# Kernel tuning notes

Hardware: AMD Instinct MI355X
Metric: run time of the kernel (lower is better)

The kernel has to match this reference:

```python
import jax, jax.numpy as jnp
import numpy as np

HIDDEN = 1024
INTER = 4096
NUM_EXPERTS = 8
TOP_K = 2


def setup_inputs() -> dict:
    key = jax.random.key(0)
    ks = jax.random.split(key, 6)
    B, S = 4, 2048
    hidden_states = jax.random.normal(ks[0], (B, S, HIDDEN), dtype=jnp.float32)
    scale = 0.02
    # nn.Linear stores weight as [out, in]; y = x @ W.T + b
    gate_w = jax.random.normal(ks[1], (NUM_EXPERTS, HIDDEN), dtype=jnp.float32) * scale
    W1 = jax.random.normal(ks[2], (NUM_EXPERTS, INTER, HIDDEN), dtype=jnp.float32) * scale
    b1 = jax.random.normal(ks[3], (NUM_EXPERTS, INTER), dtype=jnp.float32) * scale
    W2 = jax.random.normal(ks[4], (NUM_EXPERTS, HIDDEN, INTER), dtype=jnp.float32) * scale
    b2 = jax.random.normal(ks[5], (NUM_EXPERTS, HIDDEN), dtype=jnp.float32) * scale
    return {"hidden_states": hidden_states, "gate_w": gate_w,
            "W1": W1, "b1": b1, "W2": W2, "b2": b2}


def reference(hidden_states, gate_w, W1, b1, W2, b2):
    B, S, H = hidden_states.shape
    x = hidden_states.reshape(-1, H)                      # [T, H]
    # Gating: top-k logits -> softmax over the k selected experts only
    gate_logits = x @ gate_w.T                            # [T, E]
    top_vals, top_idx = jax.lax.top_k(gate_logits, TOP_K) # [T, K]
    weights = jax.nn.softmax(top_vals, axis=-1)           # [T, K]
    # Per-token combine weight for each expert (0 if not selected)
    one_hot = jax.nn.one_hot(top_idx, NUM_EXPERTS, dtype=x.dtype)  # [T, K, E]
    combine = jnp.einsum("tk,tke->te", weights, one_hot)           # [T, E]
    # Expert MLPs: fixed small loop over experts (structurally distinct params)
    out = jnp.zeros_like(x)
    for e in range(NUM_EXPERTS):
        h = jax.nn.gelu(x @ W1[e].T + b1[e], approximate=False)  # [T, INTER]
        y = h @ W2[e].T + b2[e]                                   # [T, H]
        out = out + combine[:, e:e + 1] * y
    return out.reshape(B, S, H)
```

## Files before the change

kernel.cpp:

```cpp
#include <hip/hip_runtime.h>
#include <hip/hip_bf16.h>
#include <stdint.h>

#define HID 1024
#define INTER_ 4096
#define NE 8
#define NTOK 8192
#define NPAIR (NTOK * 2)
#define MAXT 72

using f32x4 = __attribute__((ext_vector_type(4))) float;
using bf16x8 = __attribute__((ext_vector_type(8))) __bf16;
using ushort8v = __attribute__((ext_vector_type(8))) unsigned short;

__device__ __forceinline__ unsigned short f2b(float f) {
  unsigned int u = __float_as_uint(f);
  u += 0x7fffu + ((u >> 16) & 1u);
  return (unsigned short)(u >> 16);
}
__device__ __forceinline__ float b2f(unsigned short u) {
  return __uint_as_float((unsigned int)u << 16);
}

__device__ __forceinline__ float gelu_f(float v) {
  float z = fabsf(v) * 0.70710678118654752f;
  float t = __builtin_amdgcn_rcpf(1.f + 0.3275911f * z);
  float p = t * (0.254829592f +
            t * (-0.284496736f +
            t * (1.421413741f +
            t * (-1.453152027f + t * 1.061405429f))));
  float er = 1.f - p * __expf(-z * z);
  er = copysignf(er, v);
  return 0.5f * v * (1.f + er);
}

#define GLD_LDS(gp, lp)                                                        \
  __builtin_amdgcn_global_load_lds(                                            \
      (const __attribute__((address_space(1))) unsigned int*)(const void*)(gp),\
      (__attribute__((address_space(3))) unsigned int*)(void*)(lp), 16, 0, 0)

#define WAITV(N) asm volatile("s_waitcnt vmcnt(" #N ")" ::: "memory")

__global__ __launch_bounds__(256) void gate_kernel(
    const float* __restrict__ x, const float* __restrict__ gw,
    int* __restrict__ topi, float* __restrict__ topw,
    unsigned short* __restrict__ xb)
{
  int gwave = (blockIdx.x * 256 + threadIdx.x) >> 6;
  int lane = threadIdx.x & 63;
  if (gwave >= NTOK) return;
  const float* xr = x + (size_t)gwave * HID;
  unsigned short* xo = xb + (size_t)gwave * HID;
  float acc[NE];
#pragma unroll
  for (int e = 0; e < NE; ++e) acc[e] = 0.f;
#pragma unroll
  for (int q = 0; q < 4; ++q) {
    float4 v = *reinterpret_cast<const float4*>(xr + q * 256 + lane * 4);
    ushort4 uv;
    uv.x = f2b(v.x); uv.y = f2b(v.y); uv.z = f2b(v.z); uv.w = f2b(v.w);
    *reinterpret_cast<ushort4*>(xo + q * 256 + lane * 4) = uv;
#pragma unroll
    for (int e = 0; e < NE; ++e) {
      float4 wv = *reinterpret_cast<const float4*>(gw + e * HID + q * 256 + lane * 4);
      acc[e] += v.x * wv.x + v.y * wv.y + v.z * wv.z + v.w * wv.w;
    }
  }
#pragma unroll
  for (int e = 0; e < NE; ++e) {
#pragma unroll
    for (int off = 32; off > 0; off >>= 1) acc[e] += __shfl_xor(acc[e], off);
  }
  if (lane == 0) {
    float v0 = -1e30f; int i0 = 0;
#pragma unroll
    for (int e = 0; e < NE; ++e) if (acc[e] > v0) { v0 = acc[e]; i0 = e; }
    float v1 = -1e30f; int i1 = 0;
#pragma unroll
    for (int e = 0; e < NE; ++e) if (e != i0 && acc[e] > v1) { v1 = acc[e]; i1 = e; }
    float e1 = __expf(v1 - v0);
    float s = 1.f + e1;
    topi[gwave * 2] = i0; topi[gwave * 2 + 1] = i1;
    topw[gwave * 2] = 1.f / s; topw[gwave * 2 + 1] = e1 / s;
  }
}

__global__ __launch_bounds__(256) void hist_kernel(const int* __restrict__ topi,
                                                   int* __restrict__ bcnt)
{
  int tid = threadIdx.x, blk = blockIdx.x;
  int t = blk * 256 + tid;
  int e0 = topi[t * 2], e1 = topi[t * 2 + 1];
  int w = tid >> 6, lane = tid & 63;
  __shared__ int wcnt[4][NE];
#pragma unroll
  for (int e = 0; e < NE; ++e) {
    unsigned long long m0 = __ballot(e0 == e);
    unsigned long long m1 = __ballot(e1 == e);
    if (lane == 0) wcnt[w][e] = __popcll(m0) + __popcll(m1);
  }
  __syncthreads();
  if (tid < NE) {
    int s = 0;
#pragma unroll
    for (int w2 = 0; w2 < 4; ++w2) s += wcnt[w2][tid];
    bcnt[blk * NE + tid] = s;
  }
}

__global__ void scan2_kernel(const int* __restrict__ bcnt, int* __restrict__ offs,
                             int* __restrict__ tile_e, int* __restrict__ tile_m,
                             int* __restrict__ ntile, int* __restrict__ gbase)
{
  __shared__ int cnts[NE];
  __shared__ int soffs[NE];
  int tid = threadIdx.x;
  if (tid < NE) {
    int s = 0;
#pragma unroll
    for (int b = 0; b < 32; ++b) s += bcnt[b * NE + tid];
    cnts[tid] = s;
  }
  __syncthreads();
  if (tid == 0) {
    int o = 0, tt = 0;
    for (int e = 0; e < NE; ++e) {
      offs[e] = o; soffs[e] = o;
      int c = cnts[e];
      for (int m = 0; m < c; m += 256) { tile_e[tt] = e; tile_m[tt] = m; ++tt; }
      o += c;
    }
    offs[NE] = o;
    *ntile = tt;
  }
  __syncthreads();
  if (tid < 32 * NE) {
    int b = tid >> 3, e = tid & 7;
    int g = soffs[e];
    for (int b2 = 0; b2 < b; ++b2) g += bcnt[b2 * NE + e];
    gbase[b * NE + e] = g;
  }
}

__global__ __launch_bounds__(256) void scatter2_kernel(
    const int* __restrict__ topi, const float* __restrict__ topw,
    const int* __restrict__ gbase,
    int* __restrict__ toklist, float* __restrict__ wlist, int* __restrict__ pos)
{
  int tid = threadIdx.x, blk = blockIdx.x;
  int t = blk * 256 + tid;
  int e0 = topi[t * 2], e1 = topi[t * 2 + 1];
  float w0 = topw[t * 2], w1 = topw[t * 2 + 1];
  int w = tid >> 6, lane = tid & 63;
  unsigned long long lt = (1ull << lane) - 1ull;
  unsigned long long le = lt | (1ull << lane);
  __shared__ int wcnt[4][NE];
  __shared__ int wbase[4][NE];
  int r0 = 0, r1 = 0;
#pragma unroll
  for (int e = 0; e < NE; ++e) {
    unsigned long long m0 = __ballot(e0 == e);
    unsigned long long m1 = __ballot(e1 == e);
    if (lane == 0) wcnt[w][e] = __popcll(m0) + __popcll(m1);
    if (e0 == e) r0 = __popcll(m0 & lt) + __popcll(m1 & lt);
    if (e1 == e) r1 = __popcll(m0 & le) + __popcll(m1 & lt);
  }
  __syncthreads();
  if (tid < 4 * NE) {
    int w2 = tid >> 3, e = tid & 7;
    int b = gbase[blk * NE + e];
    for (int w3 = 0; w3 < w2; ++w3) b += wcnt[w3][e];
    wbase[w2][e] = b;
  }
  __syncthreads();
  int P0 = wbase[w][e0] + r0;
  int P1 = wbase[w][e1] + r1;
  toklist[P0] = t; wlist[P0] = w0; pos[t * 2] = P0;
  toklist[P1] = t; wlist[P1] = w1; pos[t * 2 + 1] = P1;
}

__global__ __launch_bounds__(256) void cvtw_kernel(
    const float* __restrict__ W1, const float* __restrict__ W2,
    unsigned short* __restrict__ w1b, unsigned short* __restrict__ w2b, int n8)
{
  int half = gridDim.x >> 1;
  const float* src = (blockIdx.x < half) ? W1 : W2;
  unsigned short* dst = (blockIdx.x < half) ? w1b : w2b;
  int b0 = (blockIdx.x < half) ? blockIdx.x : blockIdx.x - half;
  int stride = half * 256;
  for (int i = b0 * 256 + threadIdx.x; i < n8; i += stride) {
    const float4* s = reinterpret_cast<const float4*>(src) + (size_t)i * 2;
    float4 a = s[0], b = s[1];
    ushort8v u;
    u[0] = f2b(a.x); u[1] = f2b(a.y); u[2] = f2b(a.z); u[3] = f2b(a.w);
    u[4] = f2b(b.x); u[5] = f2b(b.y); u[6] = f2b(b.z); u[7] = f2b(b.w);
    reinterpret_cast<ushort8v*>(dst)[i] = u;
  }
}


__global__ __launch_bounds__(512, 4) void gemm1_kernel(
    const unsigned short* __restrict__ xb, const unsigned short* __restrict__ w1b,
    const float* __restrict__ b1,
    const int* __restrict__ toklist, const int* __restrict__ offs,
    const int* __restrict__ tile_e, const int* __restrict__ tile_m,
    const int* __restrict__ ntile,
    unsigned short* __restrict__ hb)
{
  const int t = blockIdx.y;
  if (t >= *ntile) return;
  const int e = tile_e[t];
  const int m0 = tile_m[t];
  const int base = offs[e];
  const int cnt = offs[e + 1] - base;
  const int n0 = blockIdx.x * 128;

  __shared__ __align__(16) unsigned short As[3][256 * 32];
  __shared__ __align__(16) unsigned short Bs[3][128 * 32];

  const int tid = threadIdx.x;
  const int lane = tid & 63;
  const int w = tid >> 6;
  const int wr = w >> 1, wc = w & 1;

  const int r0 = tid >> 2;
  const int sl = tid & 3;
  const int scg = sl ^ ((r0 >> 1) & 3);
  const unsigned short* gA[2];
  const unsigned short* gB;
#pragma unroll
  for (int g = 0; g < 2; ++g) {
    int row = g * 128 + r0;
    int mrow = m0 + row; if (mrow >= cnt) mrow = cnt - 1;
    int tk = toklist[base + mrow];
    gA[g] = xb + (size_t)tk * HID + scg * 8;
  }
  gB = w1b + ((size_t)e * INTER_ + n0 + r0) * HID + scg * 8;

  int raq[4], rbq[4];
#pragma unroll
  for (int i = 0; i < 4; ++i) {
    int rA = wr * 64 + i * 16 + (lane & 15);
    raq[i] = rA * 32 + (((lane >> 4) ^ ((rA >> 1) & 3)) * 8);
    int rB = wc * 64 + i * 16 + (lane & 15);
    rbq[i] = rB * 32 + (((lane >> 4) ^ ((rB >> 1) & 3)) * 8);
  }

  f32x4 acc[4][4];
#pragma unroll
  for (int i = 0; i < 4; ++i)
#pragma unroll
    for (int j = 0; j < 4; ++j) acc[i][j] = (f32x4){0.f, 0.f, 0.f, 0.f};

  auto stage = [&](int slot, int s) {
    const int kof = s * 32;
    GLD_LDS(gA[0] + kof, &As[slot][tid * 8]);
    GLD_LDS(gA[1] + kof, &As[slot][4096 + tid * 8]);
    GLD_LDS(gB + kof,    &Bs[slot][tid * 8]);
  };
  auto compute = [&](int slot) {
    const unsigned short* Ab = &As[slot][0];
    const unsigned short* Bb = &Bs[slot][0];
    bf16x8 bfr[4];
#pragma unroll
    for (int j = 0; j < 4; ++j) bfr[j] = *reinterpret_cast<const bf16x8*>(Bb + rbq[j]);
#pragma unroll
    for (int i = 0; i < 4; ++i) {
      bf16x8 af = *reinterpret_cast<const bf16x8*>(Ab + raq[i]);
#pragma unroll
      for (int j = 0; j < 4; ++j)
        acc[i][j] = __builtin_amdgcn_mfma_f32_16x16x32_bf16(af, bfr[j], acc[i][j], 0, 0, 0);
    }
  };

  const int NS = HID / 32;
  stage(0, 0); stage(1, 1);
#pragma unroll 3
  for (int s = 0; s < NS - 2; ++s) {
    WAITV(3);
    __builtin_amdgcn_s_barrier();
    stage((s + 2) % 3, s + 2);
    compute(s % 3);
  }
  WAITV(3); __builtin_amdgcn_s_barrier(); compute((NS - 2) % 3);
  WAITV(0); __builtin_amdgcn_s_barrier(); compute((NS - 1) % 3);

  float bias[4];
  const int colb = n0 + wc * 64 + (lane & 15);
#pragma unroll
  for (int j = 0; j < 4; ++j) bias[j] = b1[(size_t)e * INTER_ + colb + j * 16];
#pragma unroll
  for (int i = 0; i < 4; ++i) {
    int mbase = m0 + wr * 64 + i * 16 + (lane >> 4) * 4;
#pragma unroll
    for (int r = 0; r < 4; ++r) {
      int m = mbase + r;
      if (m < cnt) {
        unsigned short* hrow = hb + (size_t)(base + m) * INTER_ + colb;
#pragma unroll
        for (int j = 0; j < 4; ++j)
          hrow[j * 16] = f2b(gelu_f(acc[i][j][r] + bias[j]));
      }
    }
  }
}

__global__ __launch_bounds__(512, 4) void gemm2_kernel(
    const unsigned short* __restrict__ hb, const unsigned short* __restrict__ w2b,
    const int* __restrict__ offs,
    const int* __restrict__ tile_e, const int* __restrict__ tile_m,
    const int* __restrict__ ntile,
    unsigned short* __restrict__ part)
{
  const int t = blockIdx.y;
  if (t >= *ntile) return;
  const int e = tile_e[t];
  const int m0 = tile_m[t];
  const int base = offs[e];
  const int cnt = offs[e + 1] - base;
  const int n0 = blockIdx.x * 128;
  const int kbase = blockIdx.z * (INTER_ / 2);

  __shared__ __align__(16) unsigned short As[3][256 * 32];
  __shared__ __align__(16) unsigned short Bs[3][128 * 32];

  const int tid = threadIdx.x;
  const int lane = tid & 63;
  const int w = tid >> 6;
  const int wr = w >> 1, wc = w & 1;

  const int r0 = tid >> 2;
  const int sl = tid & 3;
  const int scg = sl ^ ((r0 >> 1) & 3);
  const unsigned short* gA[2];
  const unsigned short* gB;
#pragma unroll
  for (int g = 0; g < 2; ++g) {
    int row = g * 128 + r0;
    int mrow = m0 + row; if (mrow >= cnt) mrow = cnt - 1;
    gA[g] = hb + (size_t)(base + mrow) * INTER_ + kbase + scg * 8;
  }
  gB = w2b + ((size_t)e * HID + n0 + r0) * INTER_ + kbase + scg * 8;

  int raq[4], rbq[4];
#pragma unroll
  for (int i = 0; i < 4; ++i) {
    int rA = wr * 64 + i * 16 + (lane & 15);
    raq[i] = rA * 32 + (((lane >> 4) ^ ((rA >> 1) & 3)) * 8);
    int rB = wc * 64 + i * 16 + (lane & 15);
    rbq[i] = rB * 32 + (((lane >> 4) ^ ((rB >> 1) & 3)) * 8);
  }

  f32x4 acc[4][4];
#pragma unroll
  for (int i = 0; i < 4; ++i)
#pragma unroll
    for (int j = 0; j < 4; ++j) acc[i][j] = (f32x4){0.f, 0.f, 0.f, 0.f};

  auto stage = [&](int slot, int s) {
    const int kof = s * 32;
    GLD_LDS(gA[0] + kof, &As[slot][tid * 8]);
    GLD_LDS(gA[1] + kof, &As[slot][4096 + tid * 8]);
    GLD_LDS(gB + kof,    &Bs[slot][tid * 8]);
  };
  auto compute = [&](int slot) {
    const unsigned short* Ab = &As[slot][0];
    const unsigned short* Bb = &Bs[slot][0];
    bf16x8 bfr[4];
#pragma unroll
    for (int j = 0; j < 4; ++j) bfr[j] = *reinterpret_cast<const bf16x8*>(Bb + rbq[j]);
#pragma unroll
    for (int i = 0; i < 4; ++i) {
      bf16x8 af = *reinterpret_cast<const bf16x8*>(Ab + raq[i]);
#pragma unroll
      for (int j = 0; j < 4; ++j)
        acc[i][j] = __builtin_amdgcn_mfma_f32_16x16x32_bf16(af, bfr[j], acc[i][j], 0, 0, 0);
    }
  };

  const int NS = (INTER_ / 2) / 32;
  stage(0, 0); stage(1, 1);
#pragma unroll 3
  for (int s = 0; s < NS - 2; ++s) {
    WAITV(3);
    __builtin_amdgcn_s_barrier();
    stage((s + 2) % 3, s + 2);
    compute(s % 3);
  }
  WAITV(3); __builtin_amdgcn_s_barrier(); compute((NS - 2) % 3);
  WAITV(0); __builtin_amdgcn_s_barrier(); compute((NS - 1) % 3);

  const int colb = n0 + wc * 64 + (lane & 15);
  unsigned short* pbase = part + (size_t)blockIdx.z * NPAIR * HID;
#pragma unroll
  for (int i = 0; i < 4; ++i) {
    int mbase = m0 + wr * 64 + i * 16 + (lane >> 4) * 4;
#pragma unroll
    for (int r = 0; r < 4; ++r) {
      int m = mbase + r;
      if (m < cnt) {
        unsigned short* prow = pbase + (size_t)(base + m) * HID + colb;
#pragma unroll
        for (int j = 0; j < 4; ++j)
          prow[j * 16] = f2b(acc[i][j][r]);
      }
    }
  }
}

__global__ __launch_bounds__(256) void combine_kernel(
    const unsigned short* __restrict__ part, const float* __restrict__ b2,
    const int* __restrict__ topi, const float* __restrict__ topw,
    const int* __restrict__ pos, float* __restrict__ out)
{
  int t = blockIdx.x * 4 + (threadIdx.x >> 6);
  int lane = threadIdx.x & 63;
  int c0 = lane * 16;
  float o[16];
#pragma unroll
  for (int c = 0; c < 16; ++c) o[c] = 0.f;
#pragma unroll
  for (int k = 0; k < 2; ++k) {
    int p = pos[t * 2 + k];
    int e = topi[t * 2 + k];
    float wk = topw[t * 2 + k];
    const unsigned short* rp0 = part + (size_t)p * HID + c0;
    const unsigned short* rp1 = part + ((size_t)NPAIR + p) * HID + c0;
    const float* bb = b2 + (size_t)e * HID + c0;
#pragma unroll
    for (int v = 0; v < 2; ++v) {
      ushort8v a = *reinterpret_cast<const ushort8v*>(rp0 + v * 8);
      ushort8v b = *reinterpret_cast<const ushort8v*>(rp1 + v * 8);
      float4 bb0 = *reinterpret_cast<const float4*>(bb + v * 8);
      float4 bb1 = *reinterpret_cast<const float4*>(bb + v * 8 + 4);
      o[v * 8 + 0] += wk * (b2f(a[0]) + b2f(b[0]) + bb0.x);
      o[v * 8 + 1] += wk * (b2f(a[1]) + b2f(b[1]) + bb0.y);
      o[v * 8 + 2] += wk * (b2f(a[2]) + b2f(b[2]) + bb0.z);
      o[v * 8 + 3] += wk * (b2f(a[3]) + b2f(b[3]) + bb0.w);
      o[v * 8 + 4] += wk * (b2f(a[4]) + b2f(b[4]) + bb1.x);
      o[v * 8 + 5] += wk * (b2f(a[5]) + b2f(b[5]) + bb1.y);
      o[v * 8 + 6] += wk * (b2f(a[6]) + b2f(b[6]) + bb1.z);
      o[v * 8 + 7] += wk * (b2f(a[7]) + b2f(b[7]) + bb1.w);
    }
  }
  float4* op = reinterpret_cast<float4*>(out + (size_t)t * HID + c0);
#pragma unroll
  for (int v = 0; v < 4; ++v)
    op[v] = make_float4(o[v * 4], o[v * 4 + 1], o[v * 4 + 2], o[v * 4 + 3]);
}

extern "C" void kernel_launch(void* const* d_in, const int* in_sizes, int n_in,
                              void* d_out, int out_size, void* d_ws, size_t ws_size,
                              hipStream_t stream) {
  const float* x  = (const float*)d_in[0];
  const float* gw = (const float*)d_in[1];
  const float* W1 = (const float*)d_in[2];
  const float* b1 = (const float*)d_in[3];
  const float* W2 = (const float*)d_in[4];
  const float* b2 = (const float*)d_in[5];
  float* out = (float*)d_out;

  char* ws = (char*)d_ws;
  size_t off = 0;
  auto alloc = [&](size_t bytes) -> void* {
    void* p = ws + off;
    off += (bytes + 255) & ~(size_t)255;
    return p;
  };
  unsigned short* hb   = (unsigned short*)alloc((size_t)NPAIR * INTER_ * 2);
  unsigned short* xb   = (unsigned short*)alloc((size_t)NTOK * HID * 2);
  unsigned short* w1b  = (unsigned short*)alloc((size_t)NE * INTER_ * HID * 2);
  unsigned short* w2b  = (unsigned short*)alloc((size_t)NE * HID * INTER_ * 2);
  unsigned short* part = (unsigned short*)alloc((size_t)2 * NPAIR * HID * 2);
  int*   toklist = (int*)alloc(NPAIR * 4);
  float* wlist   = (float*)alloc(NPAIR * 4);
  int*   topi    = (int*)alloc(NTOK * 2 * 4);
  float* topw    = (float*)alloc(NTOK * 2 * 4);
  int*   pos     = (int*)alloc(NTOK * 2 * 4);
  int*   bcnt    = (int*)alloc(32 * NE * 4);
  int*   gbase   = (int*)alloc(32 * NE * 4);
  int*   offs    = (int*)alloc(64);
  int*   tile_e  = (int*)alloc(MAXT * 4);
  int*   tile_m  = (int*)alloc(MAXT * 4);
  int*   ntile   = (int*)alloc(64);

  gate_kernel<<<NTOK / 4, 256, 0, stream>>>(x, gw, topi, topw, xb);
  hist_kernel<<<32, 256, 0, stream>>>(topi, bcnt);
  scan2_kernel<<<1, 256, 0, stream>>>(bcnt, offs, tile_e, tile_m, ntile, gbase);
  scatter2_kernel<<<32, 256, 0, stream>>>(topi, topw, gbase, toklist, wlist, pos);
  cvtw_kernel<<<4096, 256, 0, stream>>>(W1, W2, w1b, w2b, NE * INTER_ * HID / 8);
  gemm1_kernel<<<dim3(INTER_ / 128, MAXT), 512, 0, stream>>>(
      xb, w1b, b1, toklist, offs, tile_e, tile_m, ntile, hb);
  gemm2_kernel<<<dim3(HID / 128, MAXT, 2), 512, 0, stream>>>(
      hb, w2b, offs, tile_e, tile_m, ntile, part);
  combine_kernel<<<NTOK / 4, 256, 0, stream>>>(part, b2, topi, topw, pos, out);
}
```

Baseline: 533.7 us.

## Prefetch LDS fragments ahead of MFMAs and remap gemm2 blocks per XCD

Both grouped GEMM kernels now issue the next stage's global-to-LDS copy before the barrier. They also load the next K-slice's A/B fragments from LDS into registers right after the current MFMA batch, so LDS reads overlap matrix math. gemm2 switches to a flattened 1D grid where each XCD (blockIdx.x & 7) gets a contiguous group of 9 tiles across all N blocks. This aims to improve L2 reuse of activations and weights within a die. The cost is extra fragment registers per thread, which may lower occupancy under the 512x4 launch bound.

```diff
diff --git a/kernel.cpp b/kernel.cpp
--- a/kernel.cpp
+++ b/kernel.cpp
@@ -252,38 +252,48 @@
 #pragma unroll
     for (int j = 0; j < 4; ++j) acc[i][j] = (f32x4){0.f, 0.f, 0.f, 0.f};
 
+  bf16x8 afr[4], bfr[4];
+
   auto stage = [&](int slot, int s) {
     const int kof = s * 32;
     GLD_LDS(gA[0] + kof, &As[slot][tid * 8]);
     GLD_LDS(gA[1] + kof, &As[slot][4096 + tid * 8]);
     GLD_LDS(gB + kof,    &Bs[slot][tid * 8]);
   };
-  auto compute = [&](int slot) {
+  auto load_frags = [&](int slot) {
     const unsigned short* Ab = &As[slot][0];
     const unsigned short* Bb = &Bs[slot][0];
-    bf16x8 bfr[4];
 #pragma unroll
     for (int j = 0; j < 4; ++j) bfr[j] = *reinterpret_cast<const bf16x8*>(Bb + rbq[j]);
 #pragma unroll
-    for (int i = 0; i < 4; ++i) {
-      bf16x8 af = *reinterpret_cast<const bf16x8*>(Ab + raq[i]);
+    for (int i = 0; i < 4; ++i) afr[i] = *reinterpret_cast<const bf16x8*>(Ab + raq[i]);
+  };
+  auto mfma_step = [&]() {
+#pragma unroll
+    for (int i = 0; i < 4; ++i)
 #pragma unroll
       for (int j = 0; j < 4; ++j)
-        acc[i][j] = __builtin_amdgcn_mfma_f32_16x16x32_bf16(af, bfr[j], acc[i][j], 0, 0, 0);
-    }
+        acc[i][j] = __builtin_amdgcn_mfma_f32_16x16x32_bf16(afr[i], bfr[j], acc[i][j], 0, 0, 0);
   };
 
   const int NS = HID / 32;
   stage(0, 0); stage(1, 1);
+  WAITV(3);
+  __builtin_amdgcn_s_barrier();
+  load_frags(0);
 #pragma unroll 3
   for (int s = 0; s < NS - 2; ++s) {
+    stage((s + 2) % 3, s + 2);
     WAITV(3);
     __builtin_amdgcn_s_barrier();
-    stage((s + 2) % 3, s + 2);
-    compute(s % 3);
-  }
-  WAITV(3); __builtin_amdgcn_s_barrier(); compute((NS - 2) % 3);
-  WAITV(0); __builtin_amdgcn_s_barrier(); compute((NS - 1) % 3);
+    mfma_step();
+    load_frags((s + 1) % 3);
+  }
+  WAITV(0);
+  __builtin_amdgcn_s_barrier();
+  mfma_step();
+  load_frags((NS - 1) % 3);
+  mfma_step();
 
   float bias[4];
   const int colb = n0 + wc * 64 + (lane & 15);
@@ -312,13 +322,17 @@
     const int* __restrict__ ntile,
     unsigned short* __restrict__ part)
 {
-  const int t = blockIdx.y;
+  const int h = blockIdx.x;
+  const int xcd = h & 7;
+  const int j = h >> 3;
+  const int t = 9 * xcd + j % 9;
+  const int nb = j / 9;
   if (t >= *ntile) return;
   const int e = tile_e[t];
   const int m0 = tile_m[t];
   const int base = offs[e];
   const int cnt = offs[e + 1] - base;
-  const int n0 = blockIdx.x * 128;
+  const int n0 = nb * 128;
   const int kbase = blockIdx.z * (INTER_ / 2);
 
   __shared__ __align__(16) unsigned short As[3][256 * 32];
@@ -355,7 +369,9 @@
 #pragma unroll
   for (int i = 0; i < 4; ++i)
 #pragma unroll
-    for (int j = 0; j < 4; ++j) acc[i][j] = (f32x4){0.f, 0.f, 0.f, 0.f};
+    for (int j2 = 0; j2 < 4; ++j2) acc[i][j2] = (f32x4){0.f, 0.f, 0.f, 0.f};
+
+  bf16x8 afr[4], bfr[4];
 
   auto stage = [&](int slot, int s) {
     const int kof = s * 32;
@@ -363,32 +379,40 @@
     GLD_LDS(gA[1] + kof, &As[slot][4096 + tid * 8]);
     GLD_LDS(gB + kof,    &Bs[slot][tid * 8]);
   };
-  auto compute = [&](int slot) {
+  auto load_frags = [&](int slot) {
     const unsigned short* Ab = &As[slot][0];
     const unsigned short* Bb = &Bs[slot][0];
-    bf16x8 bfr[4];
-#pragma unroll
-    for (int j = 0; j < 4; ++j) bfr[j] = *reinterpret_cast<const bf16x8*>(Bb + rbq[j]);
-#pragma unroll
-    for (int i = 0; i < 4; ++i) {
-      bf16x8 af = *reinterpret_cast<const bf16x8*>(Ab + raq[i]);
-#pragma unroll
-      for (int j = 0; j < 4; ++j)
-        acc[i][j] = __builtin_amdgcn_mfma_f32_16x16x32_bf16(af, bfr[j], acc[i][j], 0, 0, 0);
-    }
+#pragma unroll
+    for (int j2 = 0; j2 < 4; ++j2) bfr[j2] = *reinterpret_cast<const bf16x8*>(Bb + rbq[j2]);
+#pragma unroll
+    for (int i = 0; i < 4; ++i) afr[i] = *reinterpret_cast<const bf16x8*>(Ab + raq[i]);
+  };
+  auto mfma_step = [&]() {
+#pragma unroll
+    for (int i = 0; i < 4; ++i)
+#pragma unroll
+      for (int j2 = 0; j2 < 4; ++j2)
+        acc[i][j2] = __builtin_amdgcn_mfma_f32_16x16x32_bf16(afr[i], bfr[j2], acc[i][j2], 0, 0, 0);
   };
 
   const int NS = (INTER_ / 2) / 32;
   stage(0, 0); stage(1, 1);
+  WAITV(3);
+  __builtin_amdgcn_s_barrier();
+  load_frags(0);
 #pragma unroll 3
   for (int s = 0; s < NS - 2; ++s) {
+    stage((s + 2) % 3, s + 2);
     WAITV(3);
     __builtin_amdgcn_s_barrier();
-    stage((s + 2) % 3, s + 2);
-    compute(s % 3);
-  }
-  WAITV(3); __builtin_amdgcn_s_barrier(); compute((NS - 2) % 3);
-  WAITV(0); __builtin_amdgcn_s_barrier(); compute((NS - 1) % 3);
+    mfma_step();
+    load_frags((s + 1) % 3);
+  }
+  WAITV(0);
+  __builtin_amdgcn_s_barrier();
+  mfma_step();
+  load_frags((NS - 1) % 3);
+  mfma_step();
 
   const int colb = n0 + wc * 64 + (lane & 15);
   unsigned short* pbase = part + (size_t)blockIdx.z * NPAIR * HID;
@@ -401,8 +425,8 @@
       if (m < cnt) {
         unsigned short* prow = pbase + (size_t)(base + m) * HID + colb;
 #pragma unroll
-        for (int j = 0; j < 4; ++j)
-          prow[j * 16] = f2b(acc[i][j][r]);
+        for (int j2 = 0; j2 < 4; ++j2)
+          prow[j2 * 16] = f2b(acc[i][j2][r]);
       }
     }
   }
@@ -491,7 +515,7 @@
   cvtw_kernel<<<4096, 256, 0, stream>>>(W1, W2, w1b, w2b, NE * INTER_ * HID / 8);
   gemm1_kernel<<<dim3(INTER_ / 128, MAXT), 512, 0, stream>>>(
       xb, w1b, b1, toklist, offs, tile_e, tile_m, ntile, hb);
-  gemm2_kernel<<<dim3(HID / 128, MAXT, 2), 512, 0, stream>>>(
+  gemm2_kernel<<<dim3(8 * MAXT, 1, 2), 512, 0, stream>>>(
       hb, w2b, offs, tile_e, tile_m, ntile, part);
   combine_kernel<<<NTOK / 4, 256, 0, stream>>>(part, b2, topi, topw, pos, out);
 }
```

Result: faster. 490.1 us (-8.2%).
